# Performance work log

Hardware: AMD Instinct MI355X
Metric: run time of the kernel (lower is better)

## Reference

```python
import jax, jax.numpy as jnp
import numpy as np

M, N, D_MODEL = 16, 2048, 512
H, D = 8, 64  # num_heads, head_dim; inner_dim = H*D = 512


def setup_inputs() -> dict:
    key = jax.random.key(0)
    ks = jax.random.split(key, 8)
    s = 1.0 / np.sqrt(D_MODEL)
    return {
        "xq": jax.random.normal(ks[0], (M, N, D_MODEL), jnp.float32),
        "xk": jax.random.normal(ks[1], (M, N, D_MODEL), jnp.float32),
        "xv": jax.random.normal(ks[2], (M, N, D_MODEL), jnp.float32),
        "Wq": jax.random.normal(ks[3], (D_MODEL, H * D), jnp.float32) * s,
        "Wk": jax.random.normal(ks[4], (D_MODEL, H * D), jnp.float32) * s,
        "Wv": jax.random.normal(ks[5], (D_MODEL, H * D), jnp.float32) * s,
        "Wo": jax.random.normal(ks[6], (H * D, D_MODEL), jnp.float32) * s,
        "bo": jnp.zeros((D_MODEL,), jnp.float32),
    }


def _split_heads(x):
    # [m, n, h*d] -> [m, h, n, d]
    m, n, _ = x.shape
    return x.reshape(m, n, H, D).transpose(0, 2, 1, 3)


def reference(xq, xk, xv, Wq, Wk, Wv, Wo, bo):
    scale = D ** -0.5
    q = _split_heads(xq @ Wq)
    k = _split_heads(xk @ Wk)
    v = _split_heads(xv @ Wv)
    # linear attention: softmax over feature dim for both q and k
    q = jax.nn.softmax(q, axis=-1) * scale
    k = jax.nn.softmax(k, axis=-1)
    kv = jnp.einsum('mhnd,mhne->mhde', k, v)   # [m, h, d, d]
    out = jnp.einsum('mhqd,mhde->mhqe', q, kv)  # [m, h, nq, d]
    out = out.transpose(0, 2, 1, 3).reshape(out.shape[0], -1, H * D)
    return out @ Wo + bo
```

## Files before the change

### kernel.cpp

```cpp
#include <hip/hip_runtime.h>
#include <hip/hip_bf16.h>


typedef __bf16 bf16;
typedef __bf16 bf16x8 __attribute__((ext_vector_type(8)));
typedef __bf16 bf16x4 __attribute__((ext_vector_type(4)));
typedef float  f32x4  __attribute__((ext_vector_type(4)));

#define MFMA16(a, b, c) __builtin_amdgcn_mfma_f32_16x16x32_bf16((a), (b), (c), 0, 0, 0)

__global__ __launch_bounds__(256) void k_prep(const float* __restrict__ w0, const float* __restrict__ w1,
                                              const float* __restrict__ w2, const float* __restrict__ w3,
                                              bf16* __restrict__ t0, bf16* __restrict__ t1,
                                              bf16* __restrict__ t2, bf16* __restrict__ t3)
{
  const float* W = (blockIdx.z == 0) ? w0 : (blockIdx.z == 1) ? w1 : (blockIdx.z == 2) ? w2 : w3;
  bf16*        T = (blockIdx.z == 0) ? t0 : (blockIdx.z == 1) ? t1 : (blockIdx.z == 2) ? t2 : t3;
  __shared__ float lds[64][68];
  const int t = threadIdx.x;
  const int r = t >> 2, c0 = (t & 3) << 4;
  const float* src = W + (size_t)(blockIdx.x * 64 + r) * 512 + blockIdx.y * 64 + c0;
  float4 f0 = ((const float4*)src)[0];
  float4 f1 = ((const float4*)src)[1];
  float4 f2 = ((const float4*)src)[2];
  float4 f3 = ((const float4*)src)[3];
  *(float4*)&lds[r][c0 + 0]  = f0;
  *(float4*)&lds[r][c0 + 4]  = f1;
  *(float4*)&lds[r][c0 + 8]  = f2;
  *(float4*)&lds[r][c0 + 12] = f3;
  __syncthreads();
  bf16 v[16];
#pragma unroll
  for (int s = 0; s < 16; ++s) v[s] = (bf16)lds[c0 + s][r];
  bf16* dst = T + (size_t)(blockIdx.y * 64 + r) * 512 + blockIdx.x * 64 + c0;
  *(bf16x8*)&dst[0] = *(bf16x8*)&v[0];
  *(bf16x8*)&dst[8] = *(bf16x8*)&v[8];
}

__global__ __launch_bounds__(512) void k_qkv(const float* __restrict__ xq, const float* __restrict__ xk,
                                             const float* __restrict__ xv,
                                             const bf16* __restrict__ WqT, const bf16* __restrict__ WkT,
                                             const bf16* __restrict__ WvT,
                                             bf16* __restrict__ Qo, bf16* __restrict__ Ko, bf16* __restrict__ Vo)
{
  const int proj = blockIdx.z;
  const float* X  = (proj == 0) ? xq  : (proj == 1) ? xk  : xv;
  const bf16*  WT = (proj == 0) ? WqT : (proj == 1) ? WkT : WvT;
  bf16*       OUT = (proj == 0) ? Qo  : (proj == 1) ? Ko  : Vo;

  __shared__ bf16 As[64][40];
  __shared__ bf16 Bs[512][40];

  const int t = threadIdx.x;
  const int lane = t & 63, wave = t >> 6;
  const int g = lane >> 4, li = lane & 15;
  const size_t arow = (size_t)blockIdx.x * 64;

  f32x4 acc[4][4] = {};

  const int ar = t >> 3, ac = (t & 7) << 2;
  const int br = t >> 2, bc = (t & 3) << 3;

  for (int kt = 0; kt < 16; ++kt) {
    const int k0 = kt * 32;
    __syncthreads();
    {
      float4 f = *(const float4*)(X + (arow + ar) * 512 + k0 + ac);
      bf16x4 h; h[0] = (bf16)f.x; h[1] = (bf16)f.y; h[2] = (bf16)f.z; h[3] = (bf16)f.w;
      *(bf16x4*)&As[ar][ac] = h;
    }
#pragma unroll
    for (int i = 0; i < 4; ++i) {
      const int r = br + i * 128;
      bf16x8 b = *(const bf16x8*)(WT + (size_t)r * 512 + k0 + bc);
      *(bf16x8*)&Bs[r][bc] = b;
    }
    __syncthreads();
    bf16x8 af[4], bfr[4];
#pragma unroll
    for (int rt = 0; rt < 4; ++rt) af[rt]  = *(const bf16x8*)&As[rt * 16 + li][g * 8];
#pragma unroll
    for (int ct = 0; ct < 4; ++ct) bfr[ct] = *(const bf16x8*)&Bs[wave * 64 + ct * 16 + li][g * 8];
#pragma unroll
    for (int rt = 0; rt < 4; ++rt)
#pragma unroll
      for (int ct = 0; ct < 4; ++ct)
        acc[rt][ct] = MFMA16(af[rt], bfr[ct], acc[rt][ct]);
  }

#pragma unroll
  for (int rt = 0; rt < 4; ++rt) {
#pragma unroll
    for (int q = 0; q < 4; ++q) {
      float v0 = acc[rt][0][q], v1 = acc[rt][1][q], v2 = acc[rt][2][q], v3 = acc[rt][3][q];
      if (proj < 2) {
        float mx = fmaxf(fmaxf(v0, v1), fmaxf(v2, v3));
        mx = fmaxf(mx, __shfl_xor(mx, 1));
        mx = fmaxf(mx, __shfl_xor(mx, 2));
        mx = fmaxf(mx, __shfl_xor(mx, 4));
        mx = fmaxf(mx, __shfl_xor(mx, 8));
        v0 = __expf(v0 - mx); v1 = __expf(v1 - mx); v2 = __expf(v2 - mx); v3 = __expf(v3 - mx);
        float s = v0 + v1 + v2 + v3;
        s += __shfl_xor(s, 1); s += __shfl_xor(s, 2); s += __shfl_xor(s, 4); s += __shfl_xor(s, 8);
        const float inv = (proj == 0 ? 0.125f : 1.0f) / s;
        v0 *= inv; v1 *= inv; v2 *= inv; v3 *= inv;
      }
      bf16* o = OUT + (arow + rt * 16 + g * 4 + q) * 512 + wave * 64 + li;
      o[0] = (bf16)v0; o[16] = (bf16)v1; o[32] = (bf16)v2; o[48] = (bf16)v3;
    }
  }
}

__global__ __launch_bounds__(256) void k_kv(const bf16* __restrict__ K, const bf16* __restrict__ V,
                                            float* __restrict__ kvp)
{
  const int mh = blockIdx.x, m = mh >> 3, h = mh & 7;
  const int ns = blockIdx.y;
  __shared__ bf16 Kt[64][40];
  __shared__ bf16 Vt[64][40];
  const int t = threadIdx.x, lane = t & 63, wave = t >> 6;
  const int dq = wave >> 1, eq = wave & 1;
  const int g = lane >> 4, li = lane & 15;
  const int tn = t & 31, d0 = (t >> 5) << 3;
  const size_t rowbase = (size_t)m * 2048 + ns * 512;

  f32x4 acc[2][2] = {};

  for (int nt = 0; nt < 16; ++nt) {
    __syncthreads();
    {
      bf16x8 kr = *(const bf16x8*)(K + (rowbase + nt * 32 + tn) * 512 + h * 64 + d0);
      bf16x8 vr = *(const bf16x8*)(V + (rowbase + nt * 32 + tn) * 512 + h * 64 + d0);
#pragma unroll
      for (int j = 0; j < 8; ++j) Kt[d0 + j][tn] = kr[j];
#pragma unroll
      for (int j = 0; j < 8; ++j) Vt[d0 + j][tn] = vr[j];
    }
    __syncthreads();
    bf16x8 af[2], bfr[2];
#pragma unroll
    for (int dt = 0; dt < 2; ++dt) af[dt]  = *(const bf16x8*)&Kt[dq * 32 + dt * 16 + li][g * 8];
#pragma unroll
    for (int et = 0; et < 2; ++et) bfr[et] = *(const bf16x8*)&Vt[eq * 32 + et * 16 + li][g * 8];
#pragma unroll
    for (int dt = 0; dt < 2; ++dt)
#pragma unroll
      for (int et = 0; et < 2; ++et)
        acc[dt][et] = MFMA16(af[dt], bfr[et], acc[dt][et]);
  }

  float* o = kvp + ((size_t)mh * 4 + ns) * 4096;
#pragma unroll
  for (int dt = 0; dt < 2; ++dt)
#pragma unroll
    for (int et = 0; et < 2; ++et)
#pragma unroll
      for (int q = 0; q < 4; ++q) {
        const int d = dq * 32 + dt * 16 + g * 4 + q;
        const int e = eq * 32 + et * 16 + li;
        o[d * 64 + e] = acc[dt][et][q];
      }
}

__global__ __launch_bounds__(512) void k_wfused(const float* __restrict__ kvp, const bf16* __restrict__ WoT,
                                                bf16* __restrict__ WfT)
{
  const int mh = blockIdx.x, m = mh >> 3, h = mh & 7;
  __shared__ bf16 kvs[64][72];
  const int t = threadIdx.x, lane = t & 63, wave = t >> 6;
  const int g = lane >> 4, li = lane & 15;
  {
    const int d = t >> 3, e0 = (t & 7) << 3;
    const float* p = kvp + (size_t)mh * 16384 + d * 64 + e0;
#pragma unroll
    for (int j = 0; j < 8; ++j) {
      float s = p[j] + p[4096 + j] + p[8192 + j] + p[12288 + j];
      kvs[d][e0 + j] = (bf16)s;
    }
  }
  __syncthreads();
  f32x4 acc[4][4] = {};
#pragma unroll
  for (int kk = 0; kk < 2; ++kk) {
    bf16x8 af[4], bfr[4];
#pragma unroll
    for (int rt = 0; rt < 4; ++rt) {
      const int c = wave * 64 + rt * 16 + li;
      af[rt] = *(const bf16x8*)(WoT + (size_t)c * 512 + h * 64 + kk * 32 + g * 8);
    }
#pragma unroll
    for (int ct = 0; ct < 4; ++ct)
      bfr[ct] = *(const bf16x8*)&kvs[ct * 16 + li][kk * 32 + g * 8];
#pragma unroll
    for (int rt = 0; rt < 4; ++rt)
#pragma unroll
      for (int ct = 0; ct < 4; ++ct)
        acc[rt][ct] = MFMA16(af[rt], bfr[ct], acc[rt][ct]);
  }
  bf16* o = WfT + (size_t)m * 262144;
#pragma unroll
  for (int rt = 0; rt < 4; ++rt)
#pragma unroll
    for (int ct = 0; ct < 4; ++ct)
#pragma unroll
      for (int q = 0; q < 4; ++q) {
        const int c = wave * 64 + rt * 16 + g * 4 + q;
        const int r = h * 64 + ct * 16 + li;
        o[(size_t)c * 512 + r] = (bf16)acc[rt][ct][q];
      }
}

__global__ __launch_bounds__(512) void k_out(const bf16* __restrict__ Q, const bf16* __restrict__ WfT,
                                             const float* __restrict__ bo, float* __restrict__ out)
{
  __shared__ bf16 As[64][40];
  __shared__ bf16 Bs[512][40];
  const int rb = blockIdx.x;
  const int m = rb >> 5;
  const bf16* B = WfT + (size_t)m * 262144;
  const int t = threadIdx.x, lane = t & 63, wave = t >> 6;
  const int g = lane >> 4, li = lane & 15;
  const size_t arow = (size_t)rb * 64;

  f32x4 acc[4][4] = {};
  const int ar = t >> 3, ac = (t & 7) << 2;
  const int br = t >> 2, bc = (t & 3) << 3;

  for (int kt = 0; kt < 16; ++kt) {
    const int k0 = kt * 32;
    __syncthreads();
    {
      bf16x4 a = *(const bf16x4*)(Q + (arow + ar) * 512 + k0 + ac);
      *(bf16x4*)&As[ar][ac] = a;
    }
#pragma unroll
    for (int i = 0; i < 4; ++i) {
      const int r = br + i * 128;
      bf16x8 b = *(const bf16x8*)(B + (size_t)r * 512 + k0 + bc);
      *(bf16x8*)&Bs[r][bc] = b;
    }
    __syncthreads();
    bf16x8 af[4], bfr[4];
#pragma unroll
    for (int rt = 0; rt < 4; ++rt) af[rt]  = *(const bf16x8*)&As[rt * 16 + li][g * 8];
#pragma unroll
    for (int ct = 0; ct < 4; ++ct) bfr[ct] = *(const bf16x8*)&Bs[wave * 64 + ct * 16 + li][g * 8];
#pragma unroll
    for (int rt = 0; rt < 4; ++rt)
#pragma unroll
      for (int ct = 0; ct < 4; ++ct)
        acc[rt][ct] = MFMA16(af[rt], bfr[ct], acc[rt][ct]);
  }

  float bv[4];
#pragma unroll
  for (int ct = 0; ct < 4; ++ct) bv[ct] = bo[wave * 64 + ct * 16 + li];
#pragma unroll
  for (int rt = 0; rt < 4; ++rt)
#pragma unroll
    for (int q = 0; q < 4; ++q) {
      float* o = out + (arow + rt * 16 + g * 4 + q) * 512 + wave * 64 + li;
      o[0]  = acc[rt][0][q] + bv[0];
      o[16] = acc[rt][1][q] + bv[1];
      o[32] = acc[rt][2][q] + bv[2];
      o[48] = acc[rt][3][q] + bv[3];
    }
}

extern "C" void kernel_launch(void* const* d_in, const int* in_sizes, int n_in,
                              void* d_out, int out_size, void* d_ws, size_t ws_size,
                              hipStream_t stream)
{
  const float* xq = (const float*)d_in[0];
  const float* xk = (const float*)d_in[1];
  const float* xv = (const float*)d_in[2];
  const float* Wq = (const float*)d_in[3];
  const float* Wk = (const float*)d_in[4];
  const float* Wv = (const float*)d_in[5];
  const float* Wo = (const float*)d_in[6];
  const float* bo = (const float*)d_in[7];
  float* out = (float*)d_out;

  char* ws = (char*)d_ws;
  const size_t WT_BYTES  = 512 * 512 * 2;
  const size_t QKV_BYTES = (size_t)32768 * 512 * 2;
  bf16*  WqT = (bf16*)(ws);
  bf16*  WkT = (bf16*)(ws + WT_BYTES);
  bf16*  WvT = (bf16*)(ws + 2 * WT_BYTES);
  bf16*  WoT = (bf16*)(ws + 3 * WT_BYTES);
  bf16*  Qb  = (bf16*)(ws + 4 * WT_BYTES);
  bf16*  Kb  = (bf16*)(ws + 4 * WT_BYTES + QKV_BYTES);
  bf16*  Vb  = (bf16*)(ws + 4 * WT_BYTES + 2 * QKV_BYTES);
  float* kvp = (float*)(ws + 4 * WT_BYTES + 3 * QKV_BYTES);
  bf16*  WfT = Kb;

  k_prep  <<<dim3(8, 8, 4),   256, 0, stream>>>(Wq, Wk, Wv, Wo, WqT, WkT, WvT, WoT);
  k_qkv   <<<dim3(512, 1, 3), 512, 0, stream>>>(xq, xk, xv, WqT, WkT, WvT, Qb, Kb, Vb);
  k_kv    <<<dim3(128, 4),    256, 0, stream>>>(Kb, Vb, kvp);
  k_wfused<<<dim3(128),       512, 0, stream>>>(kvp, WoT, WfT);
  k_out   <<<dim3(512),       512, 0, stream>>>(Qb, WfT, bo, out);
}
```

Measured before the change: 198.8 us.

## Pre-swizzle QKV weights into MFMA fragment layout and double-buffer X tiles

The Q/K/V weights are converted into a layout that matches the MFMA B-fragment order, so each wave loads its B fragments straight from global memory into registers instead of staging the full 512-column B tile through LDS. The QKV GEMM tile grows to 128 rows with a double-buffered LDS A tile and register prefetch of the next B fragments, which halves the number of blocks and the syncs per K step. Wo gets its own transpose kernel. The cost is higher register pressure from 32 accumulators, an extra kernel launch, and repeated global reads of B by every block.

Result: faster. 178.2 us (-10.4%).

```diff
diff --git a/kernel.cpp b/kernel.cpp
--- a/kernel.cpp
+++ b/kernel.cpp
@@ -9,13 +9,49 @@
 
 #define MFMA16(a, b, c) __builtin_amdgcn_mfma_f32_16x16x32_bf16((a), (b), (c), 0, 0, 0)
 
-__global__ __launch_bounds__(256) void k_prep(const float* __restrict__ w0, const float* __restrict__ w1,
-                                              const float* __restrict__ w2, const float* __restrict__ w3,
-                                              bf16* __restrict__ t0, bf16* __restrict__ t1,
-                                              bf16* __restrict__ t2, bf16* __restrict__ t3)
-{
-  const float* W = (blockIdx.z == 0) ? w0 : (blockIdx.z == 1) ? w1 : (blockIdx.z == 2) ? w2 : w3;
-  bf16*        T = (blockIdx.z == 0) ? t0 : (blockIdx.z == 1) ? t1 : (blockIdx.z == 2) ? t2 : t3;
+__device__ inline bf16x8 cvt8(float4 a, float4 b) {
+  bf16x8 h;
+  h[0] = (bf16)a.x; h[1] = (bf16)a.y; h[2] = (bf16)a.z; h[3] = (bf16)a.w;
+  h[4] = (bf16)b.x; h[5] = (bf16)b.y; h[6] = (bf16)b.z; h[7] = (bf16)b.w;
+  return h;
+}
+
+__global__ __launch_bounds__(256) void k_prep_frag(const float* __restrict__ w0, const float* __restrict__ w1,
+                                                   const float* __restrict__ w2,
+                                                   bf16* __restrict__ f0, bf16* __restrict__ f1,
+                                                   bf16* __restrict__ f2)
+{
+  const float* W = (blockIdx.z == 0) ? w0 : (blockIdx.z == 1) ? w1 : w2;
+  bf16*        F = (blockIdx.z == 0) ? f0 : (blockIdx.z == 1) ? f1 : f2;
+  __shared__ float lds[64][68];
+  const int t = threadIdx.x;
+  const int bx = blockIdx.x, by = blockIdx.y;
+  {
+    const int r = t >> 2, c0 = (t & 3) << 4;
+    const float* src = W + (size_t)(bx * 64 + r) * 512 + by * 64 + c0;
+    float4 a = ((const float4*)src)[0], b = ((const float4*)src)[1];
+    float4 c = ((const float4*)src)[2], d = ((const float4*)src)[3];
+    *(float4*)&lds[r][c0 + 0]  = a; *(float4*)&lds[r][c0 + 4]  = b;
+    *(float4*)&lds[r][c0 + 8]  = c; *(float4*)&lds[r][c0 + 12] = d;
+  }
+  __syncthreads();
+#pragma unroll
+  for (int it = 0; it < 2; ++it) {
+    const int ch = t + it * 256;
+    const int kc = ch >> 6, cc = ch & 63;
+    bf16x8 v;
+#pragma unroll
+    for (int j = 0; j < 8; ++j) v[j] = (bf16)lds[kc * 8 + j][cc];
+    const int cg   = by >> 1;
+    const int cb7  = ((by & 1) << 2) | (cc >> 4);
+    const int ksub = kc >> 2, g = kc & 3, li = cc & 15;
+    const size_t off = (size_t)cg * 65536 + (size_t)bx * 8192 + ksub * 4096 + cb7 * 512 + (g * 16 + li) * 8;
+    *(bf16x8*)(F + off) = v;
+  }
+}
+
+__global__ __launch_bounds__(256) void k_prep_wo(const float* __restrict__ W, bf16* __restrict__ T)
+{
   __shared__ float lds[64][68];
   const int t = threadIdx.x;
   const int r = t >> 2, c0 = (t & 3) << 4;
@@ -37,59 +73,83 @@
   *(bf16x8*)&dst[8] = *(bf16x8*)&v[8];
 }
 
-__global__ __launch_bounds__(512) void k_qkv(const float* __restrict__ xq, const float* __restrict__ xk,
-                                             const float* __restrict__ xv,
-                                             const bf16* __restrict__ WqT, const bf16* __restrict__ WkT,
-                                             const bf16* __restrict__ WvT,
-                                             bf16* __restrict__ Qo, bf16* __restrict__ Ko, bf16* __restrict__ Vo)
+__global__ __launch_bounds__(512, 2) void k_qkv(const float* __restrict__ xq, const float* __restrict__ xk,
+                                                const float* __restrict__ xv,
+                                                const bf16* __restrict__ Fq, const bf16* __restrict__ Fk,
+                                                const bf16* __restrict__ Fv,
+                                                bf16* __restrict__ Qo, bf16* __restrict__ Ko,
+                                                bf16* __restrict__ Vo)
 {
   const int proj = blockIdx.z;
-  const float* X  = (proj == 0) ? xq  : (proj == 1) ? xk  : xv;
-  const bf16*  WT = (proj == 0) ? WqT : (proj == 1) ? WkT : WvT;
-  bf16*       OUT = (proj == 0) ? Qo  : (proj == 1) ? Ko  : Vo;
-
-  __shared__ bf16 As[64][40];
-  __shared__ bf16 Bs[512][40];
-
-  const int t = threadIdx.x;
-  const int lane = t & 63, wave = t >> 6;
+  const float* X  = (proj == 0) ? xq : (proj == 1) ? xk : xv;
+  const bf16*  F  = (proj == 0) ? Fq : (proj == 1) ? Fk : Fv;
+  bf16*       OUT = (proj == 0) ? Qo : (proj == 1) ? Ko : Vo;
+
+  __shared__ bf16 As[2][128][72];
+
+  const int t = threadIdx.x, lane = t & 63, w = t >> 6;
   const int g = lane >> 4, li = lane & 15;
-  const size_t arow = (size_t)blockIdx.x * 64;
-
-  f32x4 acc[4][4] = {};
-
-  const int ar = t >> 3, ac = (t & 7) << 2;
-  const int br = t >> 2, bc = (t & 3) << 3;
-
-  for (int kt = 0; kt < 16; ++kt) {
-    const int k0 = kt * 32;
-    __syncthreads();
+  const size_t arow = (size_t)blockIdx.x * 128;
+
+  const bf16* Fw = F + (w >> 1) * 65536 + (w & 1) * 2048 + lane * 8;
+
+  const int sr = t >> 2, sc = (t & 3) << 4;
+  const float* xp0 = X + (arow + sr) * 512 + sc;
+
+  f32x4 acc[8][4] = {};
+
+  {
+    float4 xa[4];
+#pragma unroll
+    for (int i = 0; i < 4; ++i) xa[i] = ((const float4*)xp0)[i];
+    *(bf16x8*)&As[0][sr][sc]     = cvt8(xa[0], xa[1]);
+    *(bf16x8*)&As[0][sr][sc + 8] = cvt8(xa[2], xa[3]);
+  }
+  bf16x8 bfc[4];
+#pragma unroll
+  for (int ct = 0; ct < 4; ++ct) bfc[ct] = *(const bf16x8*)(Fw + ct * 512);
+  __syncthreads();
+
+  float4 xa[4];
+#pragma unroll
+  for (int hs = 0; hs < 16; ++hs) {
+    const int kt = hs >> 1, cur = kt & 1;
+    bf16x8 bfn[4];
+    if (hs < 15) {
+      const bf16* p = Fw + ((hs + 1) >> 1) * 8192 + ((hs + 1) & 1) * 4096;
+#pragma unroll
+      for (int ct = 0; ct < 4; ++ct) bfn[ct] = *(const bf16x8*)(p + ct * 512);
+    }
+    if ((hs & 1) == 0 && kt < 7) {
+#pragma unroll
+      for (int i = 0; i < 4; ++i) xa[i] = ((const float4*)(xp0 + (kt + 1) * 64))[i];
+    }
     {
-      float4 f = *(const float4*)(X + (arow + ar) * 512 + k0 + ac);
-      bf16x4 h; h[0] = (bf16)f.x; h[1] = (bf16)f.y; h[2] = (bf16)f.z; h[3] = (bf16)f.w;
-      *(bf16x4*)&As[ar][ac] = h;
-    }
-#pragma unroll
-    for (int i = 0; i < 4; ++i) {
-      const int r = br + i * 128;
-      bf16x8 b = *(const bf16x8*)(WT + (size_t)r * 512 + k0 + bc);
-      *(bf16x8*)&Bs[r][bc] = b;
-    }
-    __syncthreads();
-    bf16x8 af[4], bfr[4];
-#pragma unroll
-    for (int rt = 0; rt < 4; ++rt) af[rt]  = *(const bf16x8*)&As[rt * 16 + li][g * 8];
-#pragma unroll
-    for (int ct = 0; ct < 4; ++ct) bfr[ct] = *(const bf16x8*)&Bs[wave * 64 + ct * 16 + li][g * 8];
-#pragma unroll
-    for (int rt = 0; rt < 4; ++rt)
-#pragma unroll
-      for (int ct = 0; ct < 4; ++ct)
-        acc[rt][ct] = MFMA16(af[rt], bfr[ct], acc[rt][ct]);
-  }
-
-#pragma unroll
-  for (int rt = 0; rt < 4; ++rt) {
+      bf16x8 af[8];
+#pragma unroll
+      for (int rt = 0; rt < 8; ++rt)
+        af[rt] = *(const bf16x8*)&As[cur][rt * 16 + li][(hs & 1) * 32 + g * 8];
+#pragma unroll
+      for (int rt = 0; rt < 8; ++rt)
+#pragma unroll
+        for (int ct = 0; ct < 4; ++ct)
+          acc[rt][ct] = MFMA16(af[rt], bfc[ct], acc[rt][ct]);
+    }
+    if (hs & 1) {
+      if (kt < 7) {
+        *(bf16x8*)&As[cur ^ 1][sr][sc]     = cvt8(xa[0], xa[1]);
+        *(bf16x8*)&As[cur ^ 1][sr][sc + 8] = cvt8(xa[2], xa[3]);
+      }
+      if (hs < 15) __syncthreads();
+    }
+    if (hs < 15) {
+#pragma unroll
+      for (int ct = 0; ct < 4; ++ct) bfc[ct] = bfn[ct];
+    }
+  }
+
+#pragma unroll
+  for (int rt = 0; rt < 8; ++rt) {
 #pragma unroll
     for (int q = 0; q < 4; ++q) {
       float v0 = acc[rt][0][q], v1 = acc[rt][1][q], v2 = acc[rt][2][q], v3 = acc[rt][3][q];
@@ -105,7 +165,7 @@
         const float inv = (proj == 0 ? 0.125f : 1.0f) / s;
         v0 *= inv; v1 *= inv; v2 *= inv; v3 *= inv;
       }
-      bf16* o = OUT + (arow + rt * 16 + g * 4 + q) * 512 + wave * 64 + li;
+      bf16* o = OUT + (arow + rt * 16 + g * 4 + q) * 512 + w * 64 + li;
       o[0] = (bf16)v0; o[16] = (bf16)v1; o[32] = (bf16)v2; o[48] = (bf16)v3;
     }
   }
@@ -213,7 +273,7 @@
 __global__ __launch_bounds__(512) void k_out(const bf16* __restrict__ Q, const bf16* __restrict__ WfT,
                                              const float* __restrict__ bo, float* __restrict__ out)
 {
-  __shared__ bf16 As[64][40];
+  __shared__ bf16 As2[64][40];
   __shared__ bf16 Bs[512][40];
   const int rb = blockIdx.x;
   const int m = rb >> 5;
@@ -231,7 +291,7 @@
     __syncthreads();
     {
       bf16x4 a = *(const bf16x4*)(Q + (arow + ar) * 512 + k0 + ac);
-      *(bf16x4*)&As[ar][ac] = a;
+      *(bf16x4*)&As2[ar][ac] = a;
     }
 #pragma unroll
     for (int i = 0; i < 4; ++i) {
@@ -242,7 +302,7 @@
     __syncthreads();
     bf16x8 af[4], bfr[4];
 #pragma unroll
-    for (int rt = 0; rt < 4; ++rt) af[rt]  = *(const bf16x8*)&As[rt * 16 + li][g * 8];
+    for (int rt = 0; rt < 4; ++rt) af[rt]  = *(const bf16x8*)&As2[rt * 16 + li][g * 8];
 #pragma unroll
     for (int ct = 0; ct < 4; ++ct) bfr[ct] = *(const bf16x8*)&Bs[wave * 64 + ct * 16 + li][g * 8];
 #pragma unroll
@@ -284,9 +344,9 @@
   char* ws = (char*)d_ws;
   const size_t WT_BYTES  = 512 * 512 * 2;
   const size_t QKV_BYTES = (size_t)32768 * 512 * 2;
-  bf16*  WqT = (bf16*)(ws);
-  bf16*  WkT = (bf16*)(ws + WT_BYTES);
-  bf16*  WvT = (bf16*)(ws + 2 * WT_BYTES);
+  bf16*  WFq = (bf16*)(ws);
+  bf16*  WFk = (bf16*)(ws + WT_BYTES);
+  bf16*  WFv = (bf16*)(ws + 2 * WT_BYTES);
   bf16*  WoT = (bf16*)(ws + 3 * WT_BYTES);
   bf16*  Qb  = (bf16*)(ws + 4 * WT_BYTES);
   bf16*  Kb  = (bf16*)(ws + 4 * WT_BYTES + QKV_BYTES);
@@ -294,9 +354,10 @@
   float* kvp = (float*)(ws + 4 * WT_BYTES + 3 * QKV_BYTES);
   bf16*  WfT = Kb;
 
-  k_prep  <<<dim3(8, 8, 4),   256, 0, stream>>>(Wq, Wk, Wv, Wo, WqT, WkT, WvT, WoT);
-  k_qkv   <<<dim3(512, 1, 3), 512, 0, stream>>>(xq, xk, xv, WqT, WkT, WvT, Qb, Kb, Vb);
-  k_kv    <<<dim3(128, 4),    256, 0, stream>>>(Kb, Vb, kvp);
-  k_wfused<<<dim3(128),       512, 0, stream>>>(kvp, WoT, WfT);
-  k_out   <<<dim3(512),       512, 0, stream>>>(Qb, WfT, bo, out);
-}
+  k_prep_frag<<<dim3(8, 8, 3), 256, 0, stream>>>(Wq, Wk, Wv, WFq, WFk, WFv);
+  k_prep_wo  <<<dim3(8, 8),    256, 0, stream>>>(Wo, WoT);
+  k_qkv      <<<dim3(256, 1, 3), 512, 0, stream>>>(xq, xk, xv, WFq, WFk, WFv, Qb, Kb, Vb);
+  k_kv       <<<dim3(128, 4),  256, 0, stream>>>(Kb, Vb, kvp);
+  k_wfused   <<<dim3(128),     512, 0, stream>>>(kvp, WoT, WfT);
+  k_out      <<<dim3(512),     512, 0, stream>>>(Qb, WfT, bo, out);
+}
```

## Retile QKV projection GEMM to 128x128 tiles with direct-to-LDS weight loads

Applied to the files above, without the earlier changes.

Rewrites the QKV projection kernel to use 128x128 output tiles with 256 threads and a 64-wide K step. Weight tiles go straight to LDS through global_load_lds with an XOR swizzle, and the next fp32 activation slice is prefetched into registers while the current one is computed. A block-index remap keeps the four column blocks of the same row block on the same XCD so their repeated activation reads can hit L2. The cost is that each activation row is now fetched by four column blocks, and more registers are used per thread.

After: 224.6 us. +12.9%, slower.

```diff
diff --git a/kernel.cpp b/kernel.cpp
--- a/kernel.cpp
+++ b/kernel.cpp
@@ -8,6 +8,18 @@
 typedef float  f32x4  __attribute__((ext_vector_type(4)));
 
 #define MFMA16(a, b, c) __builtin_amdgcn_mfma_f32_16x16x32_bf16((a), (b), (c), 0, 0, 0)
+
+__device__ inline bf16x8 cvt8(float4 a, float4 b) {
+  bf16x8 h;
+  h[0] = (bf16)a.x; h[1] = (bf16)a.y; h[2] = (bf16)a.z; h[3] = (bf16)a.w;
+  h[4] = (bf16)b.x; h[5] = (bf16)b.y; h[6] = (bf16)b.z; h[7] = (bf16)b.w;
+  return h;
+}
+
+__device__ inline void glds16(const void* g, void* l) {
+  __builtin_amdgcn_global_load_lds((const __attribute__((address_space(1))) void*)g,
+                                   (__attribute__((address_space(3))) void*)l, 16, 0, 0);
+}
 
 __global__ __launch_bounds__(256) void k_prep(const float* __restrict__ w0, const float* __restrict__ w1,
                                               const float* __restrict__ w2, const float* __restrict__ w3,
@@ -37,55 +49,74 @@
   *(bf16x8*)&dst[8] = *(bf16x8*)&v[8];
 }
 
-__global__ __launch_bounds__(512) void k_qkv(const float* __restrict__ xq, const float* __restrict__ xk,
-                                             const float* __restrict__ xv,
-                                             const bf16* __restrict__ WqT, const bf16* __restrict__ WkT,
-                                             const bf16* __restrict__ WvT,
-                                             bf16* __restrict__ Qo, bf16* __restrict__ Ko, bf16* __restrict__ Vo)
-{
-  const int proj = blockIdx.z;
+__global__ __launch_bounds__(256, 3) void k_qkv(const float* __restrict__ xq, const float* __restrict__ xk,
+                                                const float* __restrict__ xv,
+                                                const bf16* __restrict__ WqT, const bf16* __restrict__ WkT,
+                                                const bf16* __restrict__ WvT,
+                                                bf16* __restrict__ Qo, bf16* __restrict__ Ko,
+                                                bf16* __restrict__ Vo)
+{
+  const int wg = blockIdx.x;
+  const int o  = (wg & 7) * 384 + (wg >> 3);
+  const int proj = o >> 10;
+  const int rem  = o & 1023;
+  const int rb   = rem >> 2, cb = rem & 3;
+
   const float* X  = (proj == 0) ? xq  : (proj == 1) ? xk  : xv;
   const bf16*  WT = (proj == 0) ? WqT : (proj == 1) ? WkT : WvT;
   bf16*       OUT = (proj == 0) ? Qo  : (proj == 1) ? Ko  : Vo;
 
-  __shared__ bf16 As[64][40];
-  __shared__ bf16 Bs[512][40];
-
-  const int t = threadIdx.x;
-  const int lane = t & 63, wave = t >> 6;
+  __shared__ bf16 As[128][72];
+  __shared__ bf16 Bs[128 * 64];
+
+  const int t = threadIdx.x, lane = t & 63, w = t >> 6;
+  const int wr = w >> 1, wc = w & 1;
   const int g = lane >> 4, li = lane & 15;
-  const size_t arow = (size_t)blockIdx.x * 64;
+
+  const int arow = t >> 1, ahalf = t & 1;
+  const float* Xp = X + (size_t)(rb * 128 + arow) * 512 + ahalf * 32;
+
+  const int bc_row = w * 32 + (lane >> 3);
+  const int bchunk = (lane & 7) ^ ((lane >> 3) & 7);
+  const bf16* Bsrc = WT + (size_t)(cb * 128 + bc_row) * 512 + bchunk * 8;
+  char* BldsBase = (char*)&Bs[0] + w * 4096;
 
   f32x4 acc[4][4] = {};
-
-  const int ar = t >> 3, ac = (t & 7) << 2;
-  const int br = t >> 2, bc = (t & 3) << 3;
-
-  for (int kt = 0; kt < 16; ++kt) {
-    const int k0 = kt * 32;
-    __syncthreads();
-    {
-      float4 f = *(const float4*)(X + (arow + ar) * 512 + k0 + ac);
-      bf16x4 h; h[0] = (bf16)f.x; h[1] = (bf16)f.y; h[2] = (bf16)f.z; h[3] = (bf16)f.w;
-      *(bf16x4*)&As[ar][ac] = h;
-    }
-#pragma unroll
-    for (int i = 0; i < 4; ++i) {
-      const int r = br + i * 128;
-      bf16x8 b = *(const bf16x8*)(WT + (size_t)r * 512 + k0 + bc);
-      *(bf16x8*)&Bs[r][bc] = b;
-    }
-    __syncthreads();
-    bf16x8 af[4], bfr[4];
-#pragma unroll
-    for (int rt = 0; rt < 4; ++rt) af[rt]  = *(const bf16x8*)&As[rt * 16 + li][g * 8];
-#pragma unroll
-    for (int ct = 0; ct < 4; ++ct) bfr[ct] = *(const bf16x8*)&Bs[wave * 64 + ct * 16 + li][g * 8];
-#pragma unroll
-    for (int rt = 0; rt < 4; ++rt)
-#pragma unroll
-      for (int ct = 0; ct < 4; ++ct)
-        acc[rt][ct] = MFMA16(af[rt], bfr[ct], acc[rt][ct]);
+  float4 xa[8];
+#pragma unroll
+  for (int i = 0; i < 8; ++i) xa[i] = ((const float4*)Xp)[i];
+
+  for (int kt = 0; kt < 8; ++kt) {
+    __syncthreads();
+#pragma unroll
+    for (int jj = 0; jj < 4; ++jj)
+      *(bf16x8*)&As[arow][ahalf * 32 + jj * 8] = cvt8(xa[2 * jj], xa[2 * jj + 1]);
+#pragma unroll
+    for (int j = 0; j < 4; ++j)
+      glds16(Bsrc + (size_t)j * 8 * 512 + kt * 64, BldsBase + j * 1024);
+    if (kt < 7) {
+#pragma unroll
+      for (int i = 0; i < 8; ++i) xa[i] = ((const float4*)(Xp + (kt + 1) * 64))[i];
+    }
+    __syncthreads();
+#pragma unroll
+    for (int ksub = 0; ksub < 2; ++ksub) {
+      bf16x8 af[4], bfr[4];
+#pragma unroll
+      for (int rt = 0; rt < 4; ++rt)
+        af[rt] = *(const bf16x8*)&As[wr * 64 + rt * 16 + li][ksub * 32 + g * 8];
+#pragma unroll
+      for (int ct = 0; ct < 4; ++ct) {
+        const int c2 = wc * 64 + ct * 16 + li;
+        const int s  = (ksub * 4 + g) ^ (li & 7);
+        bfr[ct] = *(const bf16x8*)&Bs[c2 * 64 + s * 8];
+      }
+#pragma unroll
+      for (int rt = 0; rt < 4; ++rt)
+#pragma unroll
+        for (int ct = 0; ct < 4; ++ct)
+          acc[rt][ct] = MFMA16(af[rt], bfr[ct], acc[rt][ct]);
+    }
   }
 
 #pragma unroll
@@ -105,8 +136,8 @@
         const float inv = (proj == 0 ? 0.125f : 1.0f) / s;
         v0 *= inv; v1 *= inv; v2 *= inv; v3 *= inv;
       }
-      bf16* o = OUT + (arow + rt * 16 + g * 4 + q) * 512 + wave * 64 + li;
-      o[0] = (bf16)v0; o[16] = (bf16)v1; o[32] = (bf16)v2; o[48] = (bf16)v3;
+      bf16* op = OUT + (size_t)(rb * 128 + wr * 64 + rt * 16 + g * 4 + q) * 512 + cb * 128 + wc * 64 + li;
+      op[0] = (bf16)v0; op[16] = (bf16)v1; op[32] = (bf16)v2; op[48] = (bf16)v3;
     }
   }
 }
@@ -213,8 +244,8 @@
 __global__ __launch_bounds__(512) void k_out(const bf16* __restrict__ Q, const bf16* __restrict__ WfT,
                                              const float* __restrict__ bo, float* __restrict__ out)
 {
-  __shared__ bf16 As[64][40];
-  __shared__ bf16 Bs[512][40];
+  __shared__ bf16 As2[64][40];
+  __shared__ bf16 Bs2[512][40];
   const int rb = blockIdx.x;
   const int m = rb >> 5;
   const bf16* B = WfT + (size_t)m * 262144;
@@ -231,20 +262,20 @@
     __syncthreads();
     {
       bf16x4 a = *(const bf16x4*)(Q + (arow + ar) * 512 + k0 + ac);
-      *(bf16x4*)&As[ar][ac] = a;
+      *(bf16x4*)&As2[ar][ac] = a;
     }
 #pragma unroll
     for (int i = 0; i < 4; ++i) {
       const int r = br + i * 128;
       bf16x8 b = *(const bf16x8*)(B + (size_t)r * 512 + k0 + bc);
-      *(bf16x8*)&Bs[r][bc] = b;
+      *(bf16x8*)&Bs2[r][bc] = b;
     }
     __syncthreads();
     bf16x8 af[4], bfr[4];
 #pragma unroll
-    for (int rt = 0; rt < 4; ++rt) af[rt]  = *(const bf16x8*)&As[rt * 16 + li][g * 8];
-#pragma unroll
-    for (int ct = 0; ct < 4; ++ct) bfr[ct] = *(const bf16x8*)&Bs[wave * 64 + ct * 16 + li][g * 8];
+    for (int rt = 0; rt < 4; ++rt) af[rt]  = *(const bf16x8*)&As2[rt * 16 + li][g * 8];
+#pragma unroll
+    for (int ct = 0; ct < 4; ++ct) bfr[ct] = *(const bf16x8*)&Bs2[wave * 64 + ct * 16 + li][g * 8];
 #pragma unroll
     for (int rt = 0; rt < 4; ++rt)
 #pragma unroll
@@ -294,9 +325,9 @@
   float* kvp = (float*)(ws + 4 * WT_BYTES + 3 * QKV_BYTES);
   bf16*  WfT = Kb;
 
-  k_prep  <<<dim3(8, 8, 4),   256, 0, stream>>>(Wq, Wk, Wv, Wo, WqT, WkT, WvT, WoT);
-  k_qkv   <<<dim3(512, 1, 3), 512, 0, stream>>>(xq, xk, xv, WqT, WkT, WvT, Qb, Kb, Vb);
-  k_kv    <<<dim3(128, 4),    256, 0, stream>>>(Kb, Vb, kvp);
-  k_wfused<<<dim3(128),       512, 0, stream>>>(kvp, WoT, WfT);
-  k_out   <<<dim3(512),       512, 0, stream>>>(Qb, WfT, bo, out);
-}
+  k_prep  <<<dim3(8, 8, 4), 256, 0, stream>>>(Wq, Wk, Wv, Wo, WqT, WkT, WvT, WoT);
+  k_qkv   <<<dim3(3072),    256, 0, stream>>>(xq, xk, xv, WqT, WkT, WvT, Qb, Kb, Vb);
+  k_kv    <<<dim3(128, 4),  256, 0, stream>>>(Kb, Vb, kvp);
+  k_wfused<<<dim3(128),     512, 0, stream>>>(kvp, WoT, WfT);
+  k_out   <<<dim3(512),     512, 0, stream>>>(Qb, WfT, bo, out);
+}
```

## Use direct global-to-LDS loads with XOR-swizzled layouts in QKV and output GEMMs

Applied to the files above, without the earlier changes.

Replaces the register-staged weight-tile loads in k_qkv and both operand loads in k_out with global_load_lds DMA into XOR-swizzled, unpadded LDS tiles. k_out also moves to a 64-wide K step, halving the number of barrier pairs, and k_qkv prefetches the next fp32 activation chunk into registers before the compute phase. The goal is to cut VGPR round trips and LDS bank conflicts during staging. The cost is a larger LDS footprint in k_out (about 72KB), which may lower occupancy.

Result: faster. 166.9 us (-16.1%).

```diff
diff --git a/kernel.cpp b/kernel.cpp
--- a/kernel.cpp
+++ b/kernel.cpp
@@ -8,6 +8,11 @@
 typedef float  f32x4  __attribute__((ext_vector_type(4)));
 
 #define MFMA16(a, b, c) __builtin_amdgcn_mfma_f32_16x16x32_bf16((a), (b), (c), 0, 0, 0)
+
+__device__ inline void glds16(const void* g, void* l) {
+  __builtin_amdgcn_global_load_lds((const __attribute__((address_space(1))) void*)g,
+                                   (__attribute__((address_space(3))) void*)l, 16, 0, 0);
+}
 
 __global__ __launch_bounds__(256) void k_prep(const float* __restrict__ w0, const float* __restrict__ w1,
                                               const float* __restrict__ w2, const float* __restrict__ w3,
@@ -41,7 +46,8 @@
                                              const float* __restrict__ xv,
                                              const bf16* __restrict__ WqT, const bf16* __restrict__ WkT,
                                              const bf16* __restrict__ WvT,
-                                             bf16* __restrict__ Qo, bf16* __restrict__ Ko, bf16* __restrict__ Vo)
+                                             bf16* __restrict__ Qo, bf16* __restrict__ Ko,
+                                             bf16* __restrict__ Vo)
 {
   const int proj = blockIdx.z;
   const float* X  = (proj == 0) ? xq  : (proj == 1) ? xk  : xv;
@@ -49,38 +55,42 @@
   bf16*       OUT = (proj == 0) ? Qo  : (proj == 1) ? Ko  : Vo;
 
   __shared__ bf16 As[64][40];
-  __shared__ bf16 Bs[512][40];
+  __shared__ bf16 Bs[512 * 32];
 
   const int t = threadIdx.x;
-  const int lane = t & 63, wave = t >> 6;
+  const int lane = t & 63, w = t >> 6;
   const int g = lane >> 4, li = lane & 15;
   const size_t arow = (size_t)blockIdx.x * 64;
 
+  const int ar = t >> 3, ac = (t & 7) << 2;
+  const float* xp = X + (arow + ar) * 512 + ac;
+
+  const bf16* bsrc = WT + (size_t)(w * 64 + (lane >> 2)) * 512
+                        + (((lane & 3) ^ ((lane >> 3) & 3)) << 3);
+  char* bdst = (char*)&Bs[0] + w * 4096;
+  const int bslot = g ^ ((li >> 1) & 3);
+
   f32x4 acc[4][4] = {};
-
-  const int ar = t >> 3, ac = (t & 7) << 2;
-  const int br = t >> 2, bc = (t & 3) << 3;
+  float4 xa = ((const float4*)xp)[0];
 
   for (int kt = 0; kt < 16; ++kt) {
-    const int k0 = kt * 32;
     __syncthreads();
     {
-      float4 f = *(const float4*)(X + (arow + ar) * 512 + k0 + ac);
-      bf16x4 h; h[0] = (bf16)f.x; h[1] = (bf16)f.y; h[2] = (bf16)f.z; h[3] = (bf16)f.w;
+      bf16x4 h; h[0] = (bf16)xa.x; h[1] = (bf16)xa.y; h[2] = (bf16)xa.z; h[3] = (bf16)xa.w;
       *(bf16x4*)&As[ar][ac] = h;
     }
 #pragma unroll
-    for (int i = 0; i < 4; ++i) {
-      const int r = br + i * 128;
-      bf16x8 b = *(const bf16x8*)(WT + (size_t)r * 512 + k0 + bc);
-      *(bf16x8*)&Bs[r][bc] = b;
-    }
-    __syncthreads();
+    for (int j = 0; j < 4; ++j)
+      glds16(bsrc + (size_t)j * 16 * 512 + kt * 32, bdst + j * 1024);
+    __syncthreads();
+    if (kt < 15)
+      xa = ((const float4*)(xp + (kt + 1) * 32))[0];
     bf16x8 af[4], bfr[4];
 #pragma unroll
-    for (int rt = 0; rt < 4; ++rt) af[rt]  = *(const bf16x8*)&As[rt * 16 + li][g * 8];
-#pragma unroll
-    for (int ct = 0; ct < 4; ++ct) bfr[ct] = *(const bf16x8*)&Bs[wave * 64 + ct * 16 + li][g * 8];
+    for (int rt = 0; rt < 4; ++rt) af[rt] = *(const bf16x8*)&As[rt * 16 + li][g * 8];
+#pragma unroll
+    for (int ct = 0; ct < 4; ++ct)
+      bfr[ct] = *(const bf16x8*)&Bs[(w * 64 + ct * 16 + li) * 32 + bslot * 8];
 #pragma unroll
     for (int rt = 0; rt < 4; ++rt)
 #pragma unroll
@@ -105,7 +115,7 @@
         const float inv = (proj == 0 ? 0.125f : 1.0f) / s;
         v0 *= inv; v1 *= inv; v2 *= inv; v3 *= inv;
       }
-      bf16* o = OUT + (arow + rt * 16 + g * 4 + q) * 512 + wave * 64 + li;
+      bf16* o = OUT + (arow + rt * 16 + g * 4 + q) * 512 + w * 64 + li;
       o[0] = (bf16)v0; o[16] = (bf16)v1; o[32] = (bf16)v2; o[48] = (bf16)v3;
     }
   }
@@ -213,53 +223,62 @@
 __global__ __launch_bounds__(512) void k_out(const bf16* __restrict__ Q, const bf16* __restrict__ WfT,
                                              const float* __restrict__ bo, float* __restrict__ out)
 {
-  __shared__ bf16 As[64][40];
-  __shared__ bf16 Bs[512][40];
   const int rb = blockIdx.x;
-  const int m = rb >> 5;
-  const bf16* B = WfT + (size_t)m * 262144;
-  const int t = threadIdx.x, lane = t & 63, wave = t >> 6;
+  const int m  = rb >> 5;
+  const bf16* Bm = WfT + (size_t)m * 262144;
+
+  __shared__ bf16 As[64 * 64];
+  __shared__ bf16 Bs[512 * 64];
+
+  const int t = threadIdx.x, lane = t & 63, w = t >> 6;
   const int g = lane >> 4, li = lane & 15;
   const size_t arow = (size_t)rb * 64;
 
+  const int lr = lane >> 3, ls = lane & 7;
+  const int schunk = ls ^ lr;
+  const bf16* asrc = Q  + (arow + w * 8 + lr) * 512 + schunk * 8;
+  const bf16* bsrc = Bm + (size_t)(w * 64 + lr) * 512 + schunk * 8;
+  char* adst = (char*)&As[0] + w * 1024;
+  char* bdst = (char*)&Bs[0] + w * 8192;
+
   f32x4 acc[4][4] = {};
-  const int ar = t >> 3, ac = (t & 7) << 2;
-  const int br = t >> 2, bc = (t & 3) << 3;
-
-  for (int kt = 0; kt < 16; ++kt) {
-    const int k0 = kt * 32;
-    __syncthreads();
-    {
-      bf16x4 a = *(const bf16x4*)(Q + (arow + ar) * 512 + k0 + ac);
-      *(bf16x4*)&As[ar][ac] = a;
-    }
-#pragma unroll
-    for (int i = 0; i < 4; ++i) {
-      const int r = br + i * 128;
-      bf16x8 b = *(const bf16x8*)(B + (size_t)r * 512 + k0 + bc);
-      *(bf16x8*)&Bs[r][bc] = b;
-    }
-    __syncthreads();
-    bf16x8 af[4], bfr[4];
-#pragma unroll
-    for (int rt = 0; rt < 4; ++rt) af[rt]  = *(const bf16x8*)&As[rt * 16 + li][g * 8];
-#pragma unroll
-    for (int ct = 0; ct < 4; ++ct) bfr[ct] = *(const bf16x8*)&Bs[wave * 64 + ct * 16 + li][g * 8];
-#pragma unroll
-    for (int rt = 0; rt < 4; ++rt)
-#pragma unroll
-      for (int ct = 0; ct < 4; ++ct)
-        acc[rt][ct] = MFMA16(af[rt], bfr[ct], acc[rt][ct]);
+
+  for (int kt = 0; kt < 8; ++kt) {
+    __syncthreads();
+    glds16(asrc + kt * 64, adst);
+#pragma unroll
+    for (int j = 0; j < 8; ++j)
+      glds16(bsrc + (size_t)j * 8 * 512 + kt * 64, bdst + j * 1024);
+    __syncthreads();
+#pragma unroll
+    for (int ks = 0; ks < 2; ++ks) {
+      bf16x8 af[4], bfr[4];
+#pragma unroll
+      for (int rt = 0; rt < 4; ++rt) {
+        const int r = rt * 16 + li;
+        af[rt] = *(const bf16x8*)&As[r * 64 + ((ks * 4 + g) ^ (li & 7)) * 8];
+      }
+#pragma unroll
+      for (int ct = 0; ct < 4; ++ct) {
+        const int c = w * 64 + ct * 16 + li;
+        bfr[ct] = *(const bf16x8*)&Bs[c * 64 + ((ks * 4 + g) ^ (li & 7)) * 8];
+      }
+#pragma unroll
+      for (int rt = 0; rt < 4; ++rt)
+#pragma unroll
+        for (int ct = 0; ct < 4; ++ct)
+          acc[rt][ct] = MFMA16(af[rt], bfr[ct], acc[rt][ct]);
+    }
   }
 
   float bv[4];
 #pragma unroll
-  for (int ct = 0; ct < 4; ++ct) bv[ct] = bo[wave * 64 + ct * 16 + li];
+  for (int ct = 0; ct < 4; ++ct) bv[ct] = bo[w * 64 + ct * 16 + li];
 #pragma unroll
   for (int rt = 0; rt < 4; ++rt)
 #pragma unroll
     for (int q = 0; q < 4; ++q) {
-      float* o = out + (arow + rt * 16 + g * 4 + q) * 512 + wave * 64 + li;
+      float* o = out + (arow + rt * 16 + g * 4 + q) * 512 + w * 64 + li;
       o[0]  = acc[rt][0][q] + bv[0];
       o[16] = acc[rt][1][q] + bv[1];
       o[32] = acc[rt][2][q] + bv[2];
```
